# Kernel tuning notes

Measured on AMD Instinct MI355X. Metric: run time of the kernel, lower is better.

## Reference

```python
import jax, jax.numpy as jnp
import numpy as np

N = 100000      # nodes
E = 1600000     # edges (avg degree 16)
DIM = 128       # node_input_dim == node_hidden_dim
H = 8           # num_heads
D = DIM // H    # per-head out_feats = 16
NEG_SLOPE_ATTN = 0.2   # DGL GATConv attention LeakyReLU
NEG_SLOPE_ACT = 0.01   # F.leaky_relu default (inter-layer activation)


def _leaky(x, s):
    return jnp.where(x >= 0, x, s * x)


def setup_inputs() -> dict:
    key = jax.random.key(0)
    ks = jax.random.split(key, 12)
    s = 0.1
    return {
        "n_feat": jax.random.normal(ks[0], (N, DIM), jnp.float32),
        "src": jax.random.randint(ks[1], (E,), 0, N, dtype=jnp.int32),
        "dst": jax.random.randint(ks[2], (E,), 0, N, dtype=jnp.int32),
        # layer 0 params
        "W0": jax.random.normal(ks[3], (DIM, DIM), jnp.float32) * s,
        "al0": jax.random.normal(ks[4], (H, D), jnp.float32) * s,
        "ar0": jax.random.normal(ks[5], (H, D), jnp.float32) * s,
        "b0": jnp.zeros((DIM,), jnp.float32),
        # layer 1 params
        "W1": jax.random.normal(ks[6], (DIM, DIM), jnp.float32) * s,
        "al1": jax.random.normal(ks[7], (H, D), jnp.float32) * s,
        "ar1": jax.random.normal(ks[8], (H, D), jnp.float32) * s,
        "b1": jnp.zeros((DIM,), jnp.float32),
    }


def gat_layer(h, src, dst, W, al, ar, b, apply_act):
    # h: [N, DIM] -> feat: [N, H, D]
    feat = (h @ W).reshape(N, H, D)
    el = jnp.einsum('nhd,hd->nh', feat, al)   # [N, H]
    er = jnp.einsum('nhd,hd->nh', feat, ar)   # [N, H]
    # per-edge attention logits with LeakyReLU(0.2)
    e = _leaky(el[src] + er[dst], NEG_SLOPE_ATTN)         # [E, H]
    # edge-softmax over incoming edges of each dst node (numerically stable)
    m = jax.ops.segment_max(e, dst, num_segments=N)       # [N, H]
    ee = jnp.exp(e - m[dst])                              # [E, H]
    denom = jax.ops.segment_sum(ee, dst, num_segments=N)  # [N, H]
    a = ee / denom[dst]                                   # [E, H]
    # weighted message aggregation (scatter-add to dst)
    msg = feat[src] * a[:, :, None]                       # [E, H, D]
    rst = jax.ops.segment_sum(msg, dst, num_segments=N)   # [N, H, D]
    # residual (identity since in_feats == num_heads*out_feats) + bias
    rst = rst + h.reshape(N, H, D) + b.reshape(1, H, D)
    if apply_act:
        rst = _leaky(rst, NEG_SLOPE_ACT)
    return rst.reshape(N, H * D)


def reference(n_feat, src, dst, W0, al0, ar0, b0, W1, al1, ar1, b1):
    h = gat_layer(n_feat, src, dst, W0, al0, ar0, b0, apply_act=True)
    h = gat_layer(h, src, dst, W1, al1, ar1, b1, apply_act=False)
    return h
```

## Files before the change

kernel.cpp:

```cpp
#include <hip/hip_runtime.h>
#include <hip/hip_bf16.h>

#define HGAT 8
#define DIMGAT 128
#define CAPB 4608

typedef __attribute__((ext_vector_type(8))) short short8;
typedef __attribute__((ext_vector_type(4))) float f32x4;

__device__ __forceinline__ float bf16_to_f32(unsigned int u16) {
    return __uint_as_float(u16 << 16);
}
__device__ __forceinline__ unsigned short f32_to_bf16(float x) {
    unsigned int b = __float_as_uint(x);
    b += 0x7FFFu + ((b >> 16) & 1u);
    return (unsigned short)(b >> 16);
}

__global__ void initb_kernel(int* __restrict__ bcursor, int nb) {
    int i = blockIdx.x * blockDim.x + threadIdx.x;
    if (i < nb) bcursor[i] = i * CAPB;
}

__global__ __launch_bounds__(256)
void bucket_scatter(const int* __restrict__ src, const int* __restrict__ dst,
                    int* __restrict__ bcursor, unsigned int* __restrict__ bucket_arr,
                    int e, int nb) {
    __shared__ int lcnt[400];
    __shared__ int lbase[400];
    __shared__ int lrank[400];
    int t = threadIdx.x;
    int e0 = blockIdx.x * 4096;
    for (int i = t; i < nb; i += 256) { lcnt[i] = 0; lrank[i] = 0; }
    __syncthreads();
    int myb[16]; int mys[16];
    #pragma unroll
    for (int q = 0; q < 16; ++q) {
        int i = e0 + q * 256 + t;
        int bb = -1, ss = 0;
        if (i < e) {
            int d = dst[i];
            bb = d >> 8;
            ss = (src[i] << 8) | (d & 255);
        }
        myb[q] = bb; mys[q] = ss;
        if (bb >= 0) atomicAdd(&lcnt[bb], 1);
    }
    __syncthreads();
    for (int i = t; i < nb; i += 256) {
        int c = lcnt[i];
        lbase[i] = c ? atomicAdd(&bcursor[i], c) : 0;
    }
    __syncthreads();
    #pragma unroll
    for (int q = 0; q < 16; ++q) {
        int bb = myb[q];
        if (bb >= 0) {
            int r = atomicAdd(&lrank[bb], 1);
            int pos = lbase[bb] + r;
            if (pos < (bb + 1) * CAPB)
                bucket_arr[pos] = (unsigned int)mys[q];
        }
    }
}

__global__ __launch_bounds__(256)
void bucket_finalize(const unsigned int* __restrict__ bucket_arr,
                     const int* __restrict__ bcursor, int* __restrict__ col_src,
                     int* __restrict__ start, int* __restrict__ deg, int n) {
    __shared__ int lcnt[256];
    __shared__ int lcur[256];
    int b = blockIdx.x;
    int t = threadIdx.x;
    int base = b * CAPB;
    int cnt_b = bcursor[b] - base;
    lcnt[t] = 0;
    __syncthreads();
    for (int i = t; i < cnt_b; i += 256)
        atomicAdd(&lcnt[bucket_arr[base + i] & 255u], 1);
    __syncthreads();
    int my = lcnt[t];
    for (int off = 1; off < 256; off <<= 1) {
        int v = (t >= off) ? lcnt[t - off] : 0;
        __syncthreads();
        lcnt[t] += v;
        __syncthreads();
    }
    int excl = lcnt[t] - my;
    int node = b * 256 + t;
    if (node < n) {
        start[node] = base + excl;
        deg[node] = my;
    }
    lcur[t] = excl;
    __syncthreads();
    for (int i = t; i < cnt_b; i += 256) {
        unsigned int p = bucket_arr[base + i];
        int r = atomicAdd(&lcur[p & 255u], 1);
        col_src[base + r] = (int)(p >> 8);
    }
}

__global__ __launch_bounds__(256)
void gemm_mfma_kernel(const float* __restrict__ A, const float* __restrict__ W,
                      unsigned short* __restrict__ Cb, int nrows) {
    int wave = (int)((blockIdx.x * (size_t)blockDim.x + threadIdx.x) >> 6);
    int nwaves = (int)((gridDim.x * (size_t)blockDim.x) >> 6);
    int lane = threadIdx.x & 63;
    int lr = lane & 15;
    int lg = lane >> 4;

    short8 bfrag[4][8];
    #pragma unroll
    for (int ks = 0; ks < 4; ++ks) {
        #pragma unroll
        for (int ct = 0; ct < 8; ++ct) {
            const float* wp = W + (ks * 32 + lg * 8) * 128 + ct * 16 + lr;
            short8 f;
            #pragma unroll
            for (int j = 0; j < 8; ++j) f[j] = (short)f32_to_bf16(wp[j * 128]);
            bfrag[ks][ct] = f;
        }
    }

    int ntiles = nrows >> 4;
    for (int t = wave; t < ntiles; t += nwaves) {
        const float* ap = A + (size_t)(t * 16 + lr) * 128 + lg * 8;
        f32x4 acc[8];
        #pragma unroll
        for (int ct = 0; ct < 8; ++ct) acc[ct] = (f32x4){0.f, 0.f, 0.f, 0.f};
        #pragma unroll
        for (int ks = 0; ks < 4; ++ks) {
            float4 a0 = *(const float4*)(ap + ks * 32);
            float4 a1 = *(const float4*)(ap + ks * 32 + 4);
            short8 af;
            af[0] = (short)f32_to_bf16(a0.x); af[1] = (short)f32_to_bf16(a0.y);
            af[2] = (short)f32_to_bf16(a0.z); af[3] = (short)f32_to_bf16(a0.w);
            af[4] = (short)f32_to_bf16(a1.x); af[5] = (short)f32_to_bf16(a1.y);
            af[6] = (short)f32_to_bf16(a1.z); af[7] = (short)f32_to_bf16(a1.w);
            #pragma unroll
            for (int ct = 0; ct < 8; ++ct)
                acc[ct] = __builtin_amdgcn_mfma_f32_16x16x32_bf16(af, bfrag[ks][ct], acc[ct], 0, 0, 0);
        }
        unsigned short* cp = Cb + (size_t)(t * 16 + lg * 4) * 128 + lr;
        #pragma unroll
        for (int ct = 0; ct < 8; ++ct) {
            #pragma unroll
            for (int r = 0; r < 4; ++r)
                cp[(size_t)r * 128 + ct * 16] = f32_to_bf16(acc[ct][r]);
        }
    }
}

__global__ void elr_kernel(const unsigned short* __restrict__ featb,
                           const float* __restrict__ al, const float* __restrict__ ar,
                           float* __restrict__ el, float* __restrict__ er, int n) {
    int idx = blockIdx.x * blockDim.x + threadIdx.x;
    if (idx >= n * HGAT) return;
    int h = idx & 7;
    const uint4* f4 = (const uint4*)(featb + (size_t)idx * 16);
    uint4 va = f4[0], vb = f4[1];
    unsigned int w[8] = {va.x, va.y, va.z, va.w, vb.x, vb.y, vb.z, vb.w};
    const float* a1 = al + h * 16;
    const float* a2 = ar + h * 16;
    float sl = 0.f, sr = 0.f;
    #pragma unroll
    for (int q = 0; q < 8; ++q) {
        float lo = bf16_to_f32(w[q] & 0xFFFFu);
        float hi = bf16_to_f32(w[q] >> 16);
        sl = fmaf(lo, a1[2 * q], fmaf(hi, a1[2 * q + 1], sl));
        sr = fmaf(lo, a2[2 * q], fmaf(hi, a2[2 * q + 1], sr));
    }
    el[idx] = sl;
    er[idx] = sr;
}

__global__ __launch_bounds__(256)
void agg_kernel(const unsigned short* __restrict__ featb, const float* __restrict__ el,
                const float* __restrict__ er, const int* __restrict__ col_src,
                const int* __restrict__ start_arr, const int* __restrict__ deg,
                const float* __restrict__ hin, const float* __restrict__ bias,
                float* __restrict__ out, int n, int applyAct) {
    int wid = (int)((blockIdx.x * (size_t)blockDim.x + threadIdx.x) >> 6);
    if (wid >= n) return;
    int lane = threadIdx.x & 63;
    int h = lane >> 3;
    int start = start_arr[wid];
    int end = start + deg[wid];
    float er_own = er[wid * 8 + h];

    float sum = 0.f, ax = 0.f, ay = 0.f;
    const unsigned int* featw = (const unsigned int*)featb;
    int i = start;
    for (; i + 4 <= end; i += 4) {
        int s0 = col_src[i], s1 = col_src[i + 1], s2 = col_src[i + 2], s3 = col_src[i + 3];
        float q0 = el[s0 * 8 + h], q1 = el[s1 * 8 + h];
        float q2 = el[s2 * 8 + h], q3 = el[s3 * 8 + h];
        unsigned int f0 = featw[(size_t)s0 * 64 + lane];
        unsigned int f1 = featw[(size_t)s1 * 64 + lane];
        unsigned int f2 = featw[(size_t)s2 * 64 + lane];
        unsigned int f3 = featw[(size_t)s3 * 64 + lane];
        q0 += er_own; q0 = (q0 >= 0.f) ? q0 : 0.2f * q0; float p0 = __expf(q0);
        q1 += er_own; q1 = (q1 >= 0.f) ? q1 : 0.2f * q1; float p1 = __expf(q1);
        q2 += er_own; q2 = (q2 >= 0.f) ? q2 : 0.2f * q2; float p2 = __expf(q2);
        q3 += er_own; q3 = (q3 >= 0.f) ? q3 : 0.2f * q3; float p3 = __expf(q3);
        sum += (p0 + p1) + (p2 + p3);
        ax = fmaf(p0, bf16_to_f32(f0 & 0xFFFFu), ax);
        ay = fmaf(p0, bf16_to_f32(f0 >> 16), ay);
        ax = fmaf(p1, bf16_to_f32(f1 & 0xFFFFu), ax);
        ay = fmaf(p1, bf16_to_f32(f1 >> 16), ay);
        ax = fmaf(p2, bf16_to_f32(f2 & 0xFFFFu), ax);
        ay = fmaf(p2, bf16_to_f32(f2 >> 16), ay);
        ax = fmaf(p3, bf16_to_f32(f3 & 0xFFFFu), ax);
        ay = fmaf(p3, bf16_to_f32(f3 >> 16), ay);
    }
    for (; i < end; ++i) {
        int s = col_src[i];
        float e = el[s * 8 + h] + er_own;
        e = (e >= 0.f) ? e : 0.2f * e;
        float p = __expf(e);
        sum += p;
        unsigned int fw = featw[(size_t)s * 64 + lane];
        ax = fmaf(p, bf16_to_f32(fw & 0xFFFFu), ax);
        ay = fmaf(p, bf16_to_f32(fw >> 16), ay);
    }
    float inv = (end > start) ? 1.f / sum : 0.f;
    float2 hv = ((const float2*)hin)[(size_t)wid * 64 + lane];
    float2 bv = ((const float2*)bias)[lane];
    float ox = fmaf(ax, inv, hv.x + bv.x);
    float oy = fmaf(ay, inv, hv.y + bv.y);
    if (applyAct) {
        ox = (ox >= 0.f) ? ox : 0.01f * ox;
        oy = (oy >= 0.f) ? oy : 0.01f * oy;
    }
    ((float2*)out)[(size_t)wid * 64 + lane] = make_float2(ox, oy);
}

extern "C" void kernel_launch(void* const* d_in, const int* in_sizes, int n_in,
                              void* d_out, int out_size, void* d_ws, size_t ws_size,
                              hipStream_t stream) {
    const float* n_feat = (const float*)d_in[0];
    const int*   src    = (const int*)d_in[1];
    const int*   dst    = (const int*)d_in[2];
    const float* W0  = (const float*)d_in[3];
    const float* al0 = (const float*)d_in[4];
    const float* ar0 = (const float*)d_in[5];
    const float* b0  = (const float*)d_in[6];
    const float* W1  = (const float*)d_in[7];
    const float* al1 = (const float*)d_in[8];
    const float* ar1 = (const float*)d_in[9];
    const float* b1  = (const float*)d_in[10];

    const int n = in_sizes[0] / DIMGAT;
    const int e = in_sizes[1];
    const int nb = (n + 255) >> 8;

    char* ws = (char*)d_ws;
    size_t off = 0;
    auto alloc = [&](size_t bytes) {
        void* p = ws + off;
        off += (bytes + 255) & ~(size_t)255;
        return p;
    };
    int* bcursor = (int*)alloc((size_t)nb * 4);
    int* start   = (int*)alloc((size_t)n * 4);
    int* deg     = (int*)alloc((size_t)n * 4);
    unsigned int* bucket_arr = (unsigned int*)alloc((size_t)nb * CAPB * 4);
    int* col_src = (int*)alloc((size_t)nb * CAPB * 4);
    float* el    = (float*)alloc((size_t)n * HGAT * 4);
    float* er    = (float*)alloc((size_t)n * HGAT * 4);
    unsigned short* featb = (unsigned short*)alloc((size_t)n * DIMGAT * 2);
    float* out   = (float*)d_out;

    initb_kernel<<<(nb + 255) / 256, 256, 0, stream>>>(bcursor, nb);
    bucket_scatter<<<(e + 4095) / 4096, 256, 0, stream>>>(src, dst, bcursor,
                                                          bucket_arr, e, nb);
    bucket_finalize<<<nb, 256, 0, stream>>>(bucket_arr, bcursor, col_src,
                                            start, deg, n);

    const int gemm_grid = 512;
    const int elr_grid  = (n * HGAT + 255) / 256;
    const int agg_grid  = (n * 64 + 255) / 256;

    gemm_mfma_kernel<<<gemm_grid, 256, 0, stream>>>(n_feat, W0, featb, n);
    elr_kernel<<<elr_grid, 256, 0, stream>>>(featb, al0, ar0, el, er, n);
    agg_kernel<<<agg_grid, 256, 0, stream>>>(featb, el, er, col_src, start, deg,
                                             n_feat, b0, out, n, 1);
    gemm_mfma_kernel<<<gemm_grid, 256, 0, stream>>>(out, W1, featb, n);
    elr_kernel<<<elr_grid, 256, 0, stream>>>(featb, al1, ar1, el, er, n);
    agg_kernel<<<agg_grid, 256, 0, stream>>>(featb, el, er, col_src, start, deg,
                                             out, b1, out, n, 0);
}
```

Measured before the change: 387.9 us.

## Preconvert weights to bf16 fragments, shuffle-share edge logits in aggregation, double GEMM grid

A small kernel now converts W to bf16 once, already laid out as MFMA B fragments, so each GEMM wave loads 32 short8 vectors instead of doing strided fp32 loads and conversions. The aggregation loop now handles 8 edges per step: lanes split the col_src/el loads and exp computations, then broadcast source index and weight to the head group with shuffles. This cuts redundant per-lane gathers and exps at the cost of shuffle instructions. The GEMM grid is also doubled, and two extra small kernel launches are added.

```diff
diff --git a/kernel.cpp b/kernel.cpp
--- a/kernel.cpp
+++ b/kernel.cpp
@@ -101,8 +101,21 @@
     }
 }
 
-__global__ __launch_bounds__(256)
-void gemm_mfma_kernel(const float* __restrict__ A, const float* __restrict__ W,
+__global__ void wcvt_kernel(const float* __restrict__ W, unsigned short* __restrict__ Wb) {
+    int t = blockIdx.x * blockDim.x + threadIdx.x;
+    int lane = t & 63;
+    int ct = (t >> 6) & 7;
+    int ks = t >> 9;
+    int lr = lane & 15, lg = lane >> 4;
+    const float* wp = W + (ks * 32 + lg * 8) * 128 + ct * 16 + lr;
+    unsigned short o[8];
+    #pragma unroll
+    for (int j = 0; j < 8; ++j) o[j] = f32_to_bf16(wp[j * 128]);
+    *(uint4*)(Wb + (size_t)t * 8) = *(const uint4*)o;
+}
+
+__global__ __launch_bounds__(256)
+void gemm_mfma_kernel(const float* __restrict__ A, const unsigned short* __restrict__ Wb,
                       unsigned short* __restrict__ Cb, int nrows) {
     int wave = (int)((blockIdx.x * (size_t)blockDim.x + threadIdx.x) >> 6);
     int nwaves = (int)((gridDim.x * (size_t)blockDim.x) >> 6);
@@ -110,18 +123,13 @@
     int lr = lane & 15;
     int lg = lane >> 4;
 
+    const short8* wb8 = (const short8*)Wb;
     short8 bfrag[4][8];
     #pragma unroll
-    for (int ks = 0; ks < 4; ++ks) {
-        #pragma unroll
-        for (int ct = 0; ct < 8; ++ct) {
-            const float* wp = W + (ks * 32 + lg * 8) * 128 + ct * 16 + lr;
-            short8 f;
-            #pragma unroll
-            for (int j = 0; j < 8; ++j) f[j] = (short)f32_to_bf16(wp[j * 128]);
-            bfrag[ks][ct] = f;
-        }
-    }
+    for (int ks = 0; ks < 4; ++ks)
+        #pragma unroll
+        for (int ct = 0; ct < 8; ++ct)
+            bfrag[ks][ct] = wb8[(ks * 8 + ct) * 64 + lane];
 
     int ntiles = nrows >> 4;
     for (int t = wave; t < ntiles; t += nwaves) {
@@ -185,6 +193,7 @@
     if (wid >= n) return;
     int lane = threadIdx.x & 63;
     int h = lane >> 3;
+    int jbase = lane & 0x38;
     int start = start_arr[wid];
     int end = start + deg[wid];
     float er_own = er[wid * 8 + h];
@@ -192,27 +201,20 @@
     float sum = 0.f, ax = 0.f, ay = 0.f;
     const unsigned int* featw = (const unsigned int*)featb;
     int i = start;
-    for (; i + 4 <= end; i += 4) {
-        int s0 = col_src[i], s1 = col_src[i + 1], s2 = col_src[i + 2], s3 = col_src[i + 3];
-        float q0 = el[s0 * 8 + h], q1 = el[s1 * 8 + h];
-        float q2 = el[s2 * 8 + h], q3 = el[s3 * 8 + h];
-        unsigned int f0 = featw[(size_t)s0 * 64 + lane];
-        unsigned int f1 = featw[(size_t)s1 * 64 + lane];
-        unsigned int f2 = featw[(size_t)s2 * 64 + lane];
-        unsigned int f3 = featw[(size_t)s3 * 64 + lane];
-        q0 += er_own; q0 = (q0 >= 0.f) ? q0 : 0.2f * q0; float p0 = __expf(q0);
-        q1 += er_own; q1 = (q1 >= 0.f) ? q1 : 0.2f * q1; float p1 = __expf(q1);
-        q2 += er_own; q2 = (q2 >= 0.f) ? q2 : 0.2f * q2; float p2 = __expf(q2);
-        q3 += er_own; q3 = (q3 >= 0.f) ? q3 : 0.2f * q3; float p3 = __expf(q3);
-        sum += (p0 + p1) + (p2 + p3);
-        ax = fmaf(p0, bf16_to_f32(f0 & 0xFFFFu), ax);
-        ay = fmaf(p0, bf16_to_f32(f0 >> 16), ay);
-        ax = fmaf(p1, bf16_to_f32(f1 & 0xFFFFu), ax);
-        ay = fmaf(p1, bf16_to_f32(f1 >> 16), ay);
-        ax = fmaf(p2, bf16_to_f32(f2 & 0xFFFFu), ax);
-        ay = fmaf(p2, bf16_to_f32(f2 >> 16), ay);
-        ax = fmaf(p3, bf16_to_f32(f3 & 0xFFFFu), ax);
-        ay = fmaf(p3, bf16_to_f32(f3 >> 16), ay);
+    for (; i + 8 <= end; i += 8) {
+        int s_own = col_src[i + (lane & 7)];
+        float q = el[s_own * 8 + h] + er_own;
+        q = (q >= 0.f) ? q : 0.2f * q;
+        float p_own = __expf(q);
+        #pragma unroll
+        for (int j = 0; j < 8; ++j) {
+            int sj   = __shfl(s_own, jbase + j);
+            float pj = __shfl(p_own, jbase + j);
+            sum += pj;
+            unsigned int fw = featw[(size_t)sj * 64 + lane];
+            ax = fmaf(pj, bf16_to_f32(fw & 0xFFFFu), ax);
+            ay = fmaf(pj, bf16_to_f32(fw >> 16), ay);
+        }
     }
     for (; i < end; ++i) {
         int s = col_src[i];
@@ -270,6 +272,7 @@
     float* el    = (float*)alloc((size_t)n * HGAT * 4);
     float* er    = (float*)alloc((size_t)n * HGAT * 4);
     unsigned short* featb = (unsigned short*)alloc((size_t)n * DIMGAT * 2);
+    unsigned short* Wb    = (unsigned short*)alloc((size_t)DIMGAT * DIMGAT * 2);
     float* out   = (float*)d_out;
 
     initb_kernel<<<(nb + 255) / 256, 256, 0, stream>>>(bcursor, nb);
@@ -278,15 +281,17 @@
     bucket_finalize<<<nb, 256, 0, stream>>>(bucket_arr, bcursor, col_src,
                                             start, deg, n);
 
-    const int gemm_grid = 512;
+    const int gemm_grid = 1024;
     const int elr_grid  = (n * HGAT + 255) / 256;
     const int agg_grid  = (n * 64 + 255) / 256;
 
-    gemm_mfma_kernel<<<gemm_grid, 256, 0, stream>>>(n_feat, W0, featb, n);
+    wcvt_kernel<<<8, 256, 0, stream>>>(W0, Wb);
+    gemm_mfma_kernel<<<gemm_grid, 256, 0, stream>>>(n_feat, Wb, featb, n);
     elr_kernel<<<elr_grid, 256, 0, stream>>>(featb, al0, ar0, el, er, n);
     agg_kernel<<<agg_grid, 256, 0, stream>>>(featb, el, er, col_src, start, deg,
                                              n_feat, b0, out, n, 1);
-    gemm_mfma_kernel<<<gemm_grid, 256, 0, stream>>>(out, W1, featb, n);
+    wcvt_kernel<<<8, 256, 0, stream>>>(W1, Wb);
+    gemm_mfma_kernel<<<gemm_grid, 256, 0, stream>>>(out, Wb, featb, n);
     elr_kernel<<<elr_grid, 256, 0, stream>>>(featb, al1, ar1, el, er, n);
     agg_kernel<<<agg_grid, 256, 0, stream>>>(featb, el, er, col_src, start, deg,
                                              out, b1, out, n, 0);
```

Result: no change. 388.2 us (+0.1%).
